# Kernel tuning notes

Measured on AMD Instinct MI355X. Metric: run time of the kernel, lower is better.

## Reference

```python
import jax, jax.numpy as jnp
import numpy as np

NUM = 5   # grid intervals
K = 3     # spline order


def make_grid(in_dim, num=NUM, k=K, lo=-1.0, hi=1.0):
    # pykan: linspace over [lo,hi] with num+1 knots, extended by k on each side
    g = np.linspace(lo, hi, num + 1)
    h = (g[-1] - g[0]) / num
    left = g[0] - h * np.arange(k, 0, -1)
    right = g[-1] + h * np.arange(1, k + 1)
    g = np.concatenate([left, g, right])  # (num + 2k + 1,)
    return jnp.asarray(np.broadcast_to(g, (in_dim, g.shape[0])), dtype=jnp.float32)


def b_batch(x, grid, k=K):
    # x: (B, in), grid: (in, G) -> B-spline bases (B, in, G-k-1) via Cox-de Boor
    xe = x[:, :, None]                      # (B, in, 1)
    g = grid[None]                          # (1, in, G)
    B = ((xe >= g[:, :, :-1]) & (xe < g[:, :, 1:])).astype(x.dtype)
    for ki in range(1, k + 1):
        B = ((xe - g[:, :, :-(ki + 1)]) / (g[:, :, ki:-1] - g[:, :, :-(ki + 1)]) * B[:, :, :-1]
             + (g[:, :, ki + 1:] - xe) / (g[:, :, ki + 1:] - g[:, :, 1:-ki]) * B[:, :, 1:])
    return jnp.nan_to_num(B)


def kan_layer(x, grid, coef, scale_base, scale_sp, mask, k=K):
    # x: (B, in); coef: (in, out, num+k); scales/mask: (in, out)
    base = jax.nn.silu(x)                             # (B, in)
    Bsp = b_batch(x, grid, k)                         # (B, in, num+k)
    y = jnp.einsum('bik,iok->bio', Bsp, coef)         # spline curves (B, in, out)
    y = scale_base[None] * base[:, :, None] + scale_sp[None] * y
    y = mask[None] * y
    return jnp.sum(y, axis=1)                         # (B, out)


def setup_inputs() -> dict:
    key = jax.random.key(0)
    ks = jax.random.split(key, 10)
    B, IN, HID, OUT = 4096, 1024, 256, 128
    KC = NUM + K  # coef count per edge
    x = jax.random.normal(ks[0], (B, IN), dtype=jnp.float32)
    W1 = jax.random.normal(ks[1], (HID, IN), dtype=jnp.float32) / np.sqrt(IN)
    b1 = jnp.zeros((HID,), dtype=jnp.float32)
    grid1 = make_grid(HID)
    coef1 = jax.random.normal(ks[2], (HID, HID, KC), dtype=jnp.float32) * 0.1
    sb1 = jax.random.normal(ks[3], (HID, HID), dtype=jnp.float32) / np.sqrt(HID)
    sp1 = jnp.ones((HID, HID), dtype=jnp.float32) / np.sqrt(HID)
    mask1 = jnp.ones((HID, HID), dtype=jnp.float32)
    grid2 = make_grid(HID)
    coef2 = jax.random.normal(ks[4], (HID, OUT, KC), dtype=jnp.float32) * 0.1
    sb2 = jax.random.normal(ks[5], (HID, OUT), dtype=jnp.float32) / np.sqrt(HID)
    sp2 = jnp.ones((HID, OUT), dtype=jnp.float32) / np.sqrt(HID)
    mask2 = jnp.ones((HID, OUT), dtype=jnp.float32)
    return {"x": x, "W1": W1, "b1": b1,
            "grid1": grid1, "coef1": coef1, "sb1": sb1, "sp1": sp1, "mask1": mask1,
            "grid2": grid2, "coef2": coef2, "sb2": sb2, "sp2": sp2, "mask2": mask2}


def reference(x, W1, b1, grid1, coef1, sb1, sp1, mask1, grid2, coef2, sb2, sp2, mask2):
    h = x @ W1.T + b1                                  # fc1
    h = kan_layer(h, grid1, coef1, sb1, sp1, mask1)    # kanl1
    out = kan_layer(h, grid2, coef2, sb2, sp2, mask2)  # kanl2
    return out
```

## Files before the change

kernel.cpp:

```cpp
#include <hip/hip_runtime.h>
#include <math.h>

typedef unsigned short u16;
typedef u16 u16x4 __attribute__((ext_vector_type(4)));
typedef u16 u16x8 __attribute__((ext_vector_type(8)));
typedef float f32x4 __attribute__((ext_vector_type(4)));
typedef float f32x16 __attribute__((ext_vector_type(16)));
typedef __bf16 bf16x8 __attribute__((ext_vector_type(8)));

#define KC 8
#define K2L 2304

__device__ __forceinline__ u16 f2bf_rne(float f) {
  unsigned u = __float_as_uint(f);
  u += 0x7FFFu + ((u >> 16) & 1u);
  return (u16)(u >> 16);
}

__device__ __forceinline__ void gload16(const u16* g, u16* l) {
  __builtin_amdgcn_global_load_lds(
      (const __attribute__((address_space(1))) unsigned*)g,
      (__attribute__((address_space(3))) unsigned*)l, 16, 0, 0);
}
template <int N>
__device__ __forceinline__ void vmwait() {
  if constexpr (N == 0)      asm volatile("s_waitcnt vmcnt(0)" ::: "memory");
  else if constexpr (N == 3) asm volatile("s_waitcnt vmcnt(3)" ::: "memory");
  else if constexpr (N == 4) asm volatile("s_waitcnt vmcnt(4)" ::: "memory");
  else if constexpr (N == 6) asm volatile("s_waitcnt vmcnt(6)" ::: "memory");
  else if constexpr (N == 8) asm volatile("s_waitcnt vmcnt(8)" ::: "memory");
  else static_assert(N == 0, "unsupported vmcnt literal");
}

__device__ __forceinline__ void split4hi(const float* X, u16* hi, int i) {
  f32x4 v = ((const f32x4*)X)[i];
  u16x4 h;
#pragma unroll
  for (int c = 0; c < 4; ++c) h[c] = f2bf_rne(v[c]);
  ((u16x4*)hi)[i] = h;
}
__device__ __forceinline__ void wc_one(const float* coef, const float* sb, const float* sp,
                                       const float* mask, u16* W, int N, int idx) {
  int o = idx / K2L;
  int r = idx - o * K2L;
  int i = r / 9;
  int c = r - i * 9;
  int io = i * N + o;
  float m = mask[io];
  float v = (c == 0) ? m * sb[io] : m * sp[io] * coef[(size_t)io * KC + (c - 1)];
  W[idx] = f2bf_rne(v);
}

__global__ void prep_kernel(const float* __restrict__ x, const float* __restrict__ W1,
                            const float* __restrict__ coef1, const float* __restrict__ sb1,
                            const float* __restrict__ sp1, const float* __restrict__ mask1,
                            const float* __restrict__ coef2, const float* __restrict__ sb2,
                            const float* __restrict__ sp2, const float* __restrict__ mask2,
                            u16* __restrict__ xs_hi, u16* __restrict__ w1_hi,
                            u16* __restrict__ wc1, u16* __restrict__ wc2) {
  const int b = blockIdx.x, tid = threadIdx.x;
  if (b < 4096) {
    split4hi(x, xs_hi, b * 256 + tid);
  } else if (b < 4096 + 256) {
    split4hi(W1, w1_hi, (b - 4096) * 256 + tid);
  } else if (b < 4096 + 256 + 2304) {
    wc_one(coef1, sb1, sp1, mask1, wc1, 256, (b - 4352) * 256 + tid);
  } else {
    wc_one(coef2, sb2, sp2, mask2, wc2, 128, (b - 6656) * 256 + tid);
  }
}

struct Spl {
  float g[12];
  float d1[11], d2[10], d3[9];
};
__device__ __forceinline__ void spl_init(const float* __restrict__ grid, Spl& sp) {
#pragma unroll
  for (int j = 0; j < 12; ++j) sp.g[j] = grid[j];
#pragma unroll
  for (int j = 0; j < 11; ++j) sp.d1[j] = 1.0f / (sp.g[j + 1] - sp.g[j]);
#pragma unroll
  for (int j = 0; j < 10; ++j) sp.d2[j] = 1.0f / (sp.g[j + 2] - sp.g[j]);
#pragma unroll
  for (int j = 0; j < 9; ++j) sp.d3[j] = 1.0f / (sp.g[j + 3] - sp.g[j]);
}
__device__ __forceinline__ void expand_one(float v, const Spl& sp, u16* dst) {
  float Bv[11];
#pragma unroll
  for (int j = 0; j < 11; ++j) Bv[j] = (v >= sp.g[j] && v < sp.g[j + 1]) ? 1.0f : 0.0f;
#pragma unroll
  for (int j = 0; j < 10; ++j)
    Bv[j] = (v - sp.g[j]) * sp.d1[j] * Bv[j] + (sp.g[j + 2] - v) * sp.d1[j + 1] * Bv[j + 1];
#pragma unroll
  for (int j = 0; j < 9; ++j)
    Bv[j] = (v - sp.g[j]) * sp.d2[j] * Bv[j] + (sp.g[j + 3] - v) * sp.d2[j + 1] * Bv[j + 1];
#pragma unroll
  for (int j = 0; j < 8; ++j)
    Bv[j] = (v - sp.g[j]) * sp.d3[j] * Bv[j] + (sp.g[j + 4] - v) * sp.d3[j + 1] * Bv[j + 1];
  dst[0] = f2bf_rne(v / (1.0f + __expf(-v)));
#pragma unroll
  for (int k = 0; k < 8; ++k) dst[1 + k] = f2bf_rne(Bv[k]);
}

template <int MQ, int NQ, int KG, bool EXPAND>
__global__ __launch_bounds__(512) void gemmW(
    const u16* __restrict__ A0, const u16* __restrict__ B0,
    const float* __restrict__ bias, const float* __restrict__ grid,
    void* __restrict__ outv, int M, int N, int K, int nsteps) {
  static_assert(MQ * NQ * KG == 8, "8 waves");
  constexpr int BM = MQ * 32, BN = NQ * 32;
  constexpr int ASZ = BM * 128;
  constexpr int BUF_U16 = (BM + BN) * 128;
  constexpr int LPT = (BM + BN) * 16 / 512;
  constexpr int SPK = 8 / KG;
  __shared__ __align__(16) u16 smu[4 * BUF_U16];

  const int tid = threadIdx.x;
  const int lane = tid & 63;
  const int wid = tid >> 6;
  const int q = wid % (MQ * NQ);
  const int kg = wid / (MQ * NQ);
  const int mq = (NQ == 2) ? (q >> 1) : q;
  const int nq = (NQ == 2) ? (q & 1) : 0;

  const int nb = N / BN;
  const int nwg = (M / BM) * nb;
  const int bid = blockIdx.x;
  const int swz = (bid & 7) * (nwg >> 3) + (bid >> 3);
  const int tm = (swz / nb) * BM;
  const int tn = (swz % nb) * BN;

  const u16* pA0 = A0 + (size_t)tm * K;
  const u16* pB0 = B0 + (size_t)tn * K;

  int srcO[LPT];
  bool isA[LPT];
#pragma unroll
  for (int k = 0; k < LPT; ++k) {
    int c = tid + k * 512;
    bool a = c < BM * 16;
    int r = a ? (c >> 4) : ((c - BM * 16) >> 4);
    int sl = c & 15;
    isA[k] = a;
    srcO[k] = r * K + (((sl ^ (r & 15)) & 15) << 3);
  }

  const int lr = lane & 31;
  const int khf = lane >> 5;

  int offA[SPK], offB[SPK];
#pragma unroll
  for (int s = 0; s < SPK; ++s) {
    int slice = kg * SPK + s;
    int rowA = mq * 32 + lr;
    int rowB = nq * 32 + lr;
    offA[s] = rowA * 128 + ((((slice * 2 + khf) ^ (rowA & 15)) & 15) << 3);
    offB[s] = rowB * 128 + ((((slice * 2 + khf) ^ (rowB & 15)) & 15) << 3);
  }

  auto stage = [&](int buf, int step) {
    int kk = step << 7;
    u16* sb = smu + buf * BUF_U16;
#pragma unroll
    for (int k = 0; k < LPT; ++k)
      gload16((isA[k] ? pA0 : pB0) + srcO[k] + kk, sb + (k * 512 + wid * 64) * 8);
  };

  f32x16 acc0 = {}, acc1 = {};
  stage(0, 0);
  stage(1, 1);
  for (int i = 0; i < nsteps; ++i) {
    if (i + 2 < nsteps) {
      stage((i + 2) & 3, i + 2);
      vmwait<2 * LPT>();
    } else if (i + 1 < nsteps) {
      vmwait<LPT>();
    } else {
      vmwait<0>();
    }
    __builtin_amdgcn_sched_barrier(0);
    __builtin_amdgcn_s_barrier();
    __builtin_amdgcn_sched_barrier(0);

    const u16* sb = smu + (i & 3) * BUF_U16;
    bf16x8 af[SPK], bfr[SPK];
#pragma unroll
    for (int s = 0; s < SPK; ++s) {
      af[s] = *(const bf16x8*)(sb + offA[s]);
      bfr[s] = *(const bf16x8*)(sb + ASZ + offB[s]);
    }
#pragma unroll
    for (int s = 0; s < SPK; ++s) {
      f32x16& ac = (s & 1) ? acc1 : acc0;
      ac = __builtin_amdgcn_mfma_f32_32x32x16_bf16(af[s], bfr[s], ac, 0, 0, 0);
    }
  }
  f32x16 accv = acc0 + acc1;

  const int rbase = 4 * khf;
  const int rowq = mq * 32, colq = nq * 32;

  float* Fr = (float*)smu;
  if constexpr (KG == 2) {
    __syncthreads();
#pragma unroll
    for (int r = 0; r < 16; ++r) {
      int row = rowq + rbase + (r & 3) + 8 * (r >> 2);
      Fr[kg * (BM * BN) + row * BN + colq + lr] = accv[r];
    }
    __syncthreads();
#pragma unroll
    for (int r = 0; r < 16; ++r) {
      int row = rowq + rbase + (r & 3) + 8 * (r >> 2);
      accv[r] += Fr[(1 - kg) * (BM * BN) + row * BN + colq + lr];
    }
  } else {
    __syncthreads();
    if (kg >= 2) {
#pragma unroll
      for (int r = 0; r < 16; ++r) {
        int row = rowq + rbase + (r & 3) + 8 * (r >> 2);
        Fr[(kg - 2) * (BM * BN) + row * BN + colq + lr] = accv[r];
      }
    }
    __syncthreads();
    if (kg < 2) {
#pragma unroll
      for (int r = 0; r < 16; ++r) {
        int row = rowq + rbase + (r & 3) + 8 * (r >> 2);
        accv[r] += Fr[kg * (BM * BN) + row * BN + colq + lr];
      }
    }
    __syncthreads();
    if (kg == 1) {
#pragma unroll
      for (int r = 0; r < 16; ++r) {
        int row = rowq + rbase + (r & 3) + 8 * (r >> 2);
        Fr[row * BN + colq + lr] = accv[r];
      }
    }
    __syncthreads();
    if (kg == 0) {
#pragma unroll
      for (int r = 0; r < 16; ++r) {
        int row = rowq + rbase + (r & 3) + 8 * (r >> 2);
        accv[r] += Fr[row * BN + colq + lr];
      }
    }
  }

  if constexpr (EXPAND) {
    Spl sp;
    spl_init(grid, sp);
    __syncthreads();
    u16* Fl = smu;
    {
      int col = colq + lr;
      float bv = bias ? bias[tn + col] : 0.0f;
      const int r0 = kg * 8, r1 = r0 + 8;
#pragma unroll
      for (int r = 0; r < 16; ++r) {
        if (r >= r0 && r < r1) {
          int row = rowq + rbase + (r & 3) + 8 * (r >> 2);
          expand_one(accv[r] + bv, sp, Fl + (size_t)row * (BN * 9) + col * 9);
        }
      }
    }
    __syncthreads();
    u16* Fout = (u16*)outv;
    constexpr int RB = BN * 9 / 8;
    constexpr int CH = BM * RB;
    const size_t fstride = (size_t)N * 9;
    for (int ch = tid; ch < CH; ch += 512) {
      int r = ch / RB, o = ch - r * RB;
      *(u16x8*)(Fout + (size_t)(tm + r) * fstride + (size_t)tn * 9 + o * 8) =
          *(const u16x8*)(Fl + (size_t)ch * 8);
    }
  } else {
    if (kg == 0) {
      float* Cp = (float*)outv;
      const int cbase = tn + colq + lr;
#pragma unroll
      for (int r = 0; r < 16; ++r) {
        int row = tm + rowq + rbase + (r & 3) + 8 * (r >> 2);
        Cp[(size_t)row * N + cbase] = accv[r];
      }
    }
  }
}

extern "C" void kernel_launch(void* const* d_in, const int* in_sizes, int n_in,
                              void* d_out, int out_size, void* d_ws, size_t ws_size,
                              hipStream_t stream) {
  (void)in_sizes; (void)n_in; (void)out_size; (void)ws_size;
  const float* x     = (const float*)d_in[0];
  const float* W1    = (const float*)d_in[1];
  const float* b1    = (const float*)d_in[2];
  const float* grid1 = (const float*)d_in[3];
  const float* coef1 = (const float*)d_in[4];
  const float* sb1   = (const float*)d_in[5];
  const float* sp1   = (const float*)d_in[6];
  const float* mask1 = (const float*)d_in[7];
  const float* grid2 = (const float*)d_in[8];
  const float* coef2 = (const float*)d_in[9];
  const float* sb2   = (const float*)d_in[10];
  const float* sp2   = (const float*)d_in[11];
  const float* mask2 = (const float*)d_in[12];
  float* outp = (float*)d_out;

  char* ws = (char*)d_ws;
  size_t off = 0;
  auto alloc = [&](size_t bytes) {
    char* p = ws + off;
    off += (bytes + 255) & ~(size_t)255;
    return (void*)p;
  };
  u16* xs_hi  = (u16*)alloc((size_t)4096 * 1024 * 2);
  u16* w1_hi  = (u16*)alloc((size_t)256 * 1024 * 2);
  u16* wc1    = (u16*)alloc((size_t)256 * K2L * 2);
  u16* wc2    = (u16*)alloc((size_t)128 * K2L * 2);
  u16* F1     = (u16*)alloc((size_t)4096 * K2L * 2);
  u16* F2     = (u16*)alloc((size_t)4096 * K2L * 2);

  prep_kernel<<<7808, 256, 0, stream>>>(x, W1, coef1, sb1, sp1, mask1,
                                        coef2, sb2, sp2, mask2,
                                        xs_hi, w1_hi, wc1, wc2);

  gemmW<2, 2, 2, true><<<256, 512, 0, stream>>>(
      xs_hi, w1_hi, b1, grid1, F1, 4096, 256, 1024, 8);

  gemmW<2, 2, 2, true><<<256, 512, 0, stream>>>(
      F1, wc1, nullptr, grid2, F2, 4096, 256, 2304, 18);

  gemmW<2, 1, 4, false><<<256, 512, 0, stream>>>(
      F2, wc2, nullptr, nullptr, outp, 4096, 128, 2304, 18);
}
```

Before: 57.46 us.

## Process two K-steps per barrier with paired double-buffered LDS staging

Restructures the main GEMM loop to consume two K-steps per iteration, so each group of four LDS buffers is used as two pairs. The global-to-LDS loads for the next pair are issued right after the barrier, and each iteration then fully drains outstanding loads with vmcnt(0). The aim is to halve the number of barriers and waits per K and to give the MFMA chain larger batches of independent work. In exchange, in-flight prefetch is coarser, register use rises from holding two steps of fragments, and the loop assumes nsteps is even.

```diff
diff --git a/kernel.cpp b/kernel.cpp
--- a/kernel.cpp
+++ b/kernel.cpp
@@ -22,14 +22,8 @@
       (const __attribute__((address_space(1))) unsigned*)g,
       (__attribute__((address_space(3))) unsigned*)l, 16, 0, 0);
 }
-template <int N>
-__device__ __forceinline__ void vmwait() {
-  if constexpr (N == 0)      asm volatile("s_waitcnt vmcnt(0)" ::: "memory");
-  else if constexpr (N == 3) asm volatile("s_waitcnt vmcnt(3)" ::: "memory");
-  else if constexpr (N == 4) asm volatile("s_waitcnt vmcnt(4)" ::: "memory");
-  else if constexpr (N == 6) asm volatile("s_waitcnt vmcnt(6)" ::: "memory");
-  else if constexpr (N == 8) asm volatile("s_waitcnt vmcnt(8)" ::: "memory");
-  else static_assert(N == 0, "unsupported vmcnt literal");
+__device__ __forceinline__ void vmwait0() {
+  asm volatile("s_waitcnt vmcnt(0)" ::: "memory");
 }
 
 __device__ __forceinline__ void split4hi(const float* X, u16* hi, int i) {
@@ -169,31 +163,38 @@
   f32x16 acc0 = {}, acc1 = {};
   stage(0, 0);
   stage(1, 1);
-  for (int i = 0; i < nsteps; ++i) {
-    if (i + 2 < nsteps) {
-      stage((i + 2) & 3, i + 2);
-      vmwait<2 * LPT>();
-    } else if (i + 1 < nsteps) {
-      vmwait<LPT>();
-    } else {
-      vmwait<0>();
-    }
+  const int S2 = nsteps >> 1;
+  for (int s = 0; s < S2; ++s) {
+    vmwait0();
     __builtin_amdgcn_sched_barrier(0);
     __builtin_amdgcn_s_barrier();
     __builtin_amdgcn_sched_barrier(0);
-
-    const u16* sb = smu + (i & 3) * BUF_U16;
-    bf16x8 af[SPK], bfr[SPK];
-#pragma unroll
-    for (int s = 0; s < SPK; ++s) {
-      af[s] = *(const bf16x8*)(sb + offA[s]);
-      bfr[s] = *(const bf16x8*)(sb + ASZ + offB[s]);
-    }
-#pragma unroll
-    for (int s = 0; s < SPK; ++s) {
-      f32x16& ac = (s & 1) ? acc1 : acc0;
-      ac = __builtin_amdgcn_mfma_f32_32x32x16_bf16(af[s], bfr[s], ac, 0, 0, 0);
-    }
+    const int P = s & 1;
+    if (s + 1 < S2) {
+      stage(2 * (P ^ 1), 2 * s + 2);
+      stage(2 * (P ^ 1) + 1, 2 * s + 3);
+    }
+
+    const u16* sb0 = smu + (2 * P) * BUF_U16;
+    const u16* sb1 = smu + (2 * P + 1) * BUF_U16;
+    bf16x8 af[2][SPK], bfr[2][SPK];
+#pragma unroll
+    for (int ss = 0; ss < SPK; ++ss) {
+      af[0][ss] = *(const bf16x8*)(sb0 + offA[ss]);
+      bfr[0][ss] = *(const bf16x8*)(sb0 + ASZ + offB[ss]);
+    }
+#pragma unroll
+    for (int ss = 0; ss < SPK; ++ss) {
+      af[1][ss] = *(const bf16x8*)(sb1 + offA[ss]);
+      bfr[1][ss] = *(const bf16x8*)(sb1 + ASZ + offB[ss]);
+    }
+#pragma unroll
+    for (int j = 0; j < 2; ++j)
+#pragma unroll
+      for (int ss = 0; ss < SPK; ++ss) {
+        f32x16& ac = (ss & 1) ? acc1 : acc0;
+        ac = __builtin_amdgcn_mfma_f32_32x32x16_bf16(af[j][ss], bfr[j][ss], ac, 0, 0, 0);
+      }
   }
   f32x16 accv = acc0 + acc1;
 
```

Result: slower. 61.50 us (+7.0%).

## Fuse fp32-to-bf16 conversion of x and W1 into the first GEMM

Applied to the files above, without the earlier changes.

Removes the separate prep pass that converted x and W1 to bf16 in global memory and adds a dedicated first-layer GEMM that loads fp32 tiles from global, converts them to bf16 in registers and writes them to LDS through a register-staged pipeline. This avoids writing and rereading an 8 MB bf16 copy of x. The trade-off is twice the global read bytes per tile inside the GEMM and conversion ALU work in its main loop, in place of the async global-to-LDS loads.

```diff
diff --git a/kernel.cpp b/kernel.cpp
--- a/kernel.cpp
+++ b/kernel.cpp
@@ -32,13 +32,6 @@
   else static_assert(N == 0, "unsupported vmcnt literal");
 }
 
-__device__ __forceinline__ void split4hi(const float* X, u16* hi, int i) {
-  f32x4 v = ((const f32x4*)X)[i];
-  u16x4 h;
-#pragma unroll
-  for (int c = 0; c < 4; ++c) h[c] = f2bf_rne(v[c]);
-  ((u16x4*)hi)[i] = h;
-}
 __device__ __forceinline__ void wc_one(const float* coef, const float* sb, const float* sp,
                                        const float* mask, u16* W, int N, int idx) {
   int o = idx / K2L;
@@ -51,22 +44,16 @@
   W[idx] = f2bf_rne(v);
 }
 
-__global__ void prep_kernel(const float* __restrict__ x, const float* __restrict__ W1,
-                            const float* __restrict__ coef1, const float* __restrict__ sb1,
-                            const float* __restrict__ sp1, const float* __restrict__ mask1,
-                            const float* __restrict__ coef2, const float* __restrict__ sb2,
-                            const float* __restrict__ sp2, const float* __restrict__ mask2,
-                            u16* __restrict__ xs_hi, u16* __restrict__ w1_hi,
-                            u16* __restrict__ wc1, u16* __restrict__ wc2) {
+__global__ void prep_wc_kernel(const float* __restrict__ coef1, const float* __restrict__ sb1,
+                               const float* __restrict__ sp1, const float* __restrict__ mask1,
+                               const float* __restrict__ coef2, const float* __restrict__ sb2,
+                               const float* __restrict__ sp2, const float* __restrict__ mask2,
+                               u16* __restrict__ wc1, u16* __restrict__ wc2) {
   const int b = blockIdx.x, tid = threadIdx.x;
-  if (b < 4096) {
-    split4hi(x, xs_hi, b * 256 + tid);
-  } else if (b < 4096 + 256) {
-    split4hi(W1, w1_hi, (b - 4096) * 256 + tid);
-  } else if (b < 4096 + 256 + 2304) {
-    wc_one(coef1, sb1, sp1, mask1, wc1, 256, (b - 4352) * 256 + tid);
+  if (b < 2304) {
+    wc_one(coef1, sb1, sp1, mask1, wc1, 256, b * 256 + tid);
   } else {
-    wc_one(coef2, sb2, sp2, mask2, wc2, 128, (b - 6656) * 256 + tid);
+    wc_one(coef2, sb2, sp2, mask2, wc2, 128, (b - 2304) * 256 + tid);
   }
 }
 
@@ -286,6 +273,180 @@
         Cp[(size_t)row * N + cbase] = accv[r];
       }
     }
+  }
+}
+
+__global__ __launch_bounds__(512) void gemmL1(
+    const float* __restrict__ X, const float* __restrict__ W,
+    const float* __restrict__ bias, const float* __restrict__ grid,
+    u16* __restrict__ outF, int M, int N, int K, int nsteps) {
+  constexpr int BM = 64, BN = 64;
+  constexpr int ASZ = BM * 128;
+  constexpr int BUF_U16 = (BM + BN) * 128;
+  constexpr int SPK = 4;
+  __shared__ __align__(16) u16 smu[4 * BUF_U16];
+
+  const int tid = threadIdx.x;
+  const int lane = tid & 63;
+  const int wid = tid >> 6;
+  const int q = wid % 4;
+  const int kg = wid / 4;
+  const int mq = q >> 1, nq = q & 1;
+
+  const int nb = N / BN;
+  const int nwg = (M / BM) * nb;
+  const int bid = blockIdx.x;
+  const int swz = (bid & 7) * (nwg >> 3) + (bid >> 3);
+  const int tm = (swz / nb) * BM;
+  const int tn = (swz % nb) * BN;
+
+  const float* pX = X + (size_t)tm * K;
+  const float* pW = W + (size_t)tn * K;
+
+  int srcO[4];
+  bool isA[4];
+#pragma unroll
+  for (int k = 0; k < 4; ++k) {
+    int c = tid + k * 512;
+    bool a = c < BM * 16;
+    int r = a ? (c >> 4) : ((c - BM * 16) >> 4);
+    int sl = c & 15;
+    isA[k] = a;
+    srcO[k] = r * K + (((sl ^ (r & 15)) & 15) << 3);
+  }
+
+  const int lr = lane & 31;
+  const int khf = lane >> 5;
+  int offA[SPK], offB[SPK];
+#pragma unroll
+  for (int s = 0; s < SPK; ++s) {
+    int slice = kg * SPK + s;
+    int rowA = mq * 32 + lr;
+    int rowB = nq * 32 + lr;
+    offA[s] = rowA * 128 + ((((slice * 2 + khf) ^ (rowA & 15)) & 15) << 3);
+    offB[s] = rowB * 128 + ((((slice * 2 + khf) ^ (rowB & 15)) & 15) << 3);
+  }
+
+  f32x4 ldA[4][2], ldB[4][2];
+  auto loadsA = [&](int step) {
+#pragma unroll
+    for (int k = 0; k < 4; ++k) {
+      const float* s = (isA[k] ? pX : pW) + srcO[k] + (step << 7);
+      ldA[k][0] = *(const f32x4*)s;
+      ldA[k][1] = *(const f32x4*)(s + 4);
+    }
+  };
+  auto loadsB = [&](int step) {
+#pragma unroll
+    for (int k = 0; k < 4; ++k) {
+      const float* s = (isA[k] ? pX : pW) + srcO[k] + (step << 7);
+      ldB[k][0] = *(const f32x4*)s;
+      ldB[k][1] = *(const f32x4*)(s + 4);
+    }
+  };
+  auto writeA = [&](int buf) {
+    u16* sb = smu + buf * BUF_U16;
+#pragma unroll
+    for (int k = 0; k < 4; ++k) {
+      u16x8 h;
+#pragma unroll
+      for (int c = 0; c < 4; ++c) {
+        h[c] = f2bf_rne(ldA[k][0][c]);
+        h[c + 4] = f2bf_rne(ldA[k][1][c]);
+      }
+      *(u16x8*)(sb + (size_t)(tid + k * 512) * 8) = h;
+    }
+  };
+  auto writeB = [&](int buf) {
+    u16* sb = smu + buf * BUF_U16;
+#pragma unroll
+    for (int k = 0; k < 4; ++k) {
+      u16x8 h;
+#pragma unroll
+      for (int c = 0; c < 4; ++c) {
+        h[c] = f2bf_rne(ldB[k][0][c]);
+        h[c + 4] = f2bf_rne(ldB[k][1][c]);
+      }
+      *(u16x8*)(sb + (size_t)(tid + k * 512) * 8) = h;
+    }
+  };
+
+  loadsA(0);
+  writeA(0);
+  loadsA(1);
+  writeA(1);
+  loadsA(2);
+
+  f32x16 acc0 = {}, acc1 = {};
+  for (int i = 0; i < nsteps; ++i) {
+    if ((i & 1) == 0) {
+      if (i + 3 < nsteps) loadsB(i + 3);
+      if (i + 2 < nsteps) writeA((i + 2) & 3);
+    } else {
+      if (i + 3 < nsteps) loadsA(i + 3);
+      if (i + 2 < nsteps) writeB((i + 2) & 3);
+    }
+    asm volatile("s_waitcnt lgkmcnt(0)" ::: "memory");
+    __builtin_amdgcn_sched_barrier(0);
+    __builtin_amdgcn_s_barrier();
+    __builtin_amdgcn_sched_barrier(0);
+
+    const u16* sb = smu + (i & 3) * BUF_U16;
+    bf16x8 af[SPK], bfr[SPK];
+#pragma unroll
+    for (int s = 0; s < SPK; ++s) {
+      af[s] = *(const bf16x8*)(sb + offA[s]);
+      bfr[s] = *(const bf16x8*)(sb + ASZ + offB[s]);
+    }
+#pragma unroll
+    for (int s = 0; s < SPK; ++s) {
+      f32x16& ac = (s & 1) ? acc1 : acc0;
+      ac = __builtin_amdgcn_mfma_f32_32x32x16_bf16(af[s], bfr[s], ac, 0, 0, 0);
+    }
+  }
+  f32x16 accv = acc0 + acc1;
+
+  const int rbase = 4 * khf;
+  const int rowq = mq * 32, colq = nq * 32;
+
+  float* Fr = (float*)smu;
+  __syncthreads();
+#pragma unroll
+  for (int r = 0; r < 16; ++r) {
+    int row = rowq + rbase + (r & 3) + 8 * (r >> 2);
+    Fr[kg * (BM * BN) + row * BN + colq + lr] = accv[r];
+  }
+  __syncthreads();
+#pragma unroll
+  for (int r = 0; r < 16; ++r) {
+    int row = rowq + rbase + (r & 3) + 8 * (r >> 2);
+    accv[r] += Fr[(1 - kg) * (BM * BN) + row * BN + colq + lr];
+  }
+
+  Spl sp;
+  spl_init(grid, sp);
+  __syncthreads();
+  u16* Fl = smu;
+  {
+    int col = colq + lr;
+    float bv = bias[tn + col];
+    const int r0 = kg * 8, r1 = r0 + 8;
+#pragma unroll
+    for (int r = 0; r < 16; ++r) {
+      if (r >= r0 && r < r1) {
+        int row = rowq + rbase + (r & 3) + 8 * (r >> 2);
+        expand_one(accv[r] + bv, sp, Fl + (size_t)row * (BN * 9) + col * 9);
+      }
+    }
+  }
+  __syncthreads();
+  constexpr int RB = BN * 9 / 8;
+  constexpr int CH = BM * RB;
+  const size_t fstride = (size_t)N * 9;
+  for (int ch = tid; ch < CH; ch += 512) {
+    int r = ch / RB, o = ch - r * RB;
+    *(u16x8*)(outF + (size_t)(tm + r) * fstride + (size_t)tn * 9 + o * 8) =
+        *(const u16x8*)(Fl + (size_t)ch * 8);
   }
 }
 
@@ -315,19 +476,15 @@
     off += (bytes + 255) & ~(size_t)255;
     return (void*)p;
   };
-  u16* xs_hi  = (u16*)alloc((size_t)4096 * 1024 * 2);
-  u16* w1_hi  = (u16*)alloc((size_t)256 * 1024 * 2);
-  u16* wc1    = (u16*)alloc((size_t)256 * K2L * 2);
-  u16* wc2    = (u16*)alloc((size_t)128 * K2L * 2);
-  u16* F1     = (u16*)alloc((size_t)4096 * K2L * 2);
-  u16* F2     = (u16*)alloc((size_t)4096 * K2L * 2);
-
-  prep_kernel<<<7808, 256, 0, stream>>>(x, W1, coef1, sb1, sp1, mask1,
-                                        coef2, sb2, sp2, mask2,
-                                        xs_hi, w1_hi, wc1, wc2);
-
-  gemmW<2, 2, 2, true><<<256, 512, 0, stream>>>(
-      xs_hi, w1_hi, b1, grid1, F1, 4096, 256, 1024, 8);
+  u16* wc1 = (u16*)alloc((size_t)256 * K2L * 2);
+  u16* wc2 = (u16*)alloc((size_t)128 * K2L * 2);
+  u16* F1  = (u16*)alloc((size_t)4096 * K2L * 2);
+  u16* F2  = (u16*)alloc((size_t)4096 * K2L * 2);
+
+  prep_wc_kernel<<<3456, 256, 0, stream>>>(coef1, sb1, sp1, mask1,
+                                           coef2, sb2, sp2, mask2, wc1, wc2);
+
+  gemmL1<<<256, 512, 0, stream>>>(x, W1, b1, grid1, F1, 4096, 256, 1024, 8);
 
   gemmW<2, 2, 2, true><<<256, 512, 0, stream>>>(
       F1, wc1, nullptr, grid2, F2, 4096, 256, 2304, 18);
```

New measurement: 60.60 us. 5.5% more time.
